# Kernel optimization log

Measured on AMD Instinct MI355X. Metric: run time of the kernel, lower is better.

The kernel has to match this reference:

```python
import jax, jax.numpy as jnp
import numpy as np

NUM_HEADS = 16


def _rotate_half(x):
    x1, x2 = jnp.split(x, 2, axis=-1)
    return jnp.concatenate([-x2, x1], axis=-1)


def _rope_apply(x, sin, cos):
    return x * cos + _rotate_half(x) * sin


def setup_inputs() -> dict:
    key = jax.random.key(0)
    ks = jax.random.split(key, 6)
    B, N, C, HD = 2, 2048, 1024, 64
    x = jax.random.normal(ks[0], (B, N, C), dtype=jnp.float32)
    sin = jax.random.uniform(ks[1], (N - 1, HD), dtype=jnp.float32)
    cos = jax.random.uniform(ks[2], (N - 1, HD), dtype=jnp.float32)
    qkv_w = jax.random.normal(ks[3], (3 * C, C), dtype=jnp.float32) * (C ** -0.5)
    proj_w = jax.random.normal(ks[4], (C, C), dtype=jnp.float32) * (C ** -0.5)
    proj_b = jax.random.normal(ks[5], (C,), dtype=jnp.float32) * 0.02
    return {"x": x, "sin": sin, "cos": cos, "qkv_w": qkv_w,
            "proj_w": proj_w, "proj_b": proj_b}


def reference(x, sin, cos, qkv_w, proj_w, proj_b):
    B, N, C = x.shape
    H = NUM_HEADS
    hd = C // H
    scale = hd ** -0.5

    # QKV projection (no bias): [B,N,3C] -> [B,N,3,H,hd]
    qkv = jnp.einsum('bnc,dc->bnd', x, qkv_w).reshape(B, N, 3, H, hd)
    q = qkv[:, :, 0].transpose(0, 2, 1, 3)  # [B,H,N,hd]
    k = qkv[:, :, 1].transpose(0, 2, 1, 3)
    v = qkv[:, :, 2].transpose(0, 2, 1, 3)

    # RoPE with prefix tokens left unrotated
    prefix = N - sin.shape[0]
    q = jnp.concatenate([q[:, :, :prefix], _rope_apply(q[:, :, prefix:], sin, cos)], axis=2)
    k = jnp.concatenate([k[:, :, :prefix], _rope_apply(k[:, :, prefix:], sin, cos)], axis=2)

    # SDPA (non-causal, no mask)
    scores = jnp.einsum('bhqd,bhkd->bhqk', q, k) * scale
    attn = jax.nn.softmax(scores, axis=-1)
    o = jnp.einsum('bhqk,bhkd->bhqd', attn, v)  # [B,H,N,hd]
    o = o.transpose(0, 2, 1, 3).reshape(B, N, C)

    # Output projection
    return jnp.einsum('bnc,dc->bnd', o, proj_w) + proj_b
```

## Files before the change

kernel.cpp:

```cpp
#include <hip/hip_runtime.h>
#include <hip/hip_bf16.h>
#include <stdint.h>

typedef __hip_bfloat16 bf16;
typedef __attribute__((ext_vector_type(8))) short short8;
typedef __attribute__((ext_vector_type(4))) float floatx4;

#define DEVI static __device__ __forceinline__

typedef __attribute__((address_space(1))) const uint32_t gu32;
typedef __attribute__((address_space(3))) uint32_t lu32;

DEVI void gld_lds16(const void* g, void* l) {
    __builtin_amdgcn_global_load_lds((gu32*)g, (lu32*)l, 16, 0, 0);
}

#define QSCALE 0.18033688011112042f
#define SM_SHIFT 16.0f

__global__ void cvt3_bf16_kernel(const float* __restrict__ s0, bf16* __restrict__ d0, int n0,
                                 const float* __restrict__ s1, bf16* __restrict__ d1, int n1,
                                 const float* __restrict__ s2, bf16* __restrict__ d2, int n2) {
    int c = blockIdx.x * 256 + threadIdx.x;
    const float* src; bf16* dst;
    if (c < n0)           { src = s0; dst = d0; }
    else if (c < n0 + n1) { src = s1; dst = d1; c -= n0; }
    else if (c < n0 + n1 + n2) { src = s2; dst = d2; c -= n0 + n1; }
    else return;
    const int i = c * 4;
    float4 v = *(const float4*)(src + i);
    union { bf16 h[4]; uint2 u; } o;
    o.h[0] = __float2bfloat16(v.x);
    o.h[1] = __float2bfloat16(v.y);
    o.h[2] = __float2bfloat16(v.z);
    o.h[3] = __float2bfloat16(v.w);
    *(uint2*)(dst + i) = o.u;
}

template<int BM, int OUT_BF16, int ADD_BIAS, int SCALE_Q, int ROPE>
__global__ __launch_bounds__(256, 2) void gemm_bt_kernel(
    const bf16* __restrict__ A, const bf16* __restrict__ Bt,
    const float* __restrict__ bias, const float* __restrict__ sinp,
    const float* __restrict__ cosp, void* __restrict__ Cout,
    int M, int N, int K, int nbn)
{
    constexpr int BK = 32;
    constexpr int MFRAG = BM / 32;
    __shared__ __align__(16) bf16 As[BM * BK];
    __shared__ __align__(16) bf16 Bs[128 * BK];
    const int sb = (blockIdx.x & 7) * ((int)gridDim.x >> 3) + (blockIdx.x >> 3);
    const int bm = sb / nbn;
    const int bn = sb % nbn;
    const int lane = threadIdx.x & 63;
    const int wave = threadIdx.x >> 6;
    const int wm = (wave >> 1) * (BM / 2);
    const int wn = (wave & 1) << 6;

    const int srow0 = wave * 16 + (lane >> 2);
    const int skc = (lane & 3) * 8;
    const bf16* Ap0 = A + (size_t)(bm * BM + srow0) * K + skc;
    const bf16* Ap1 = A + (size_t)(bm * BM + srow0 + 64) * K + skc;
    const bf16* Bp0 = Bt + (size_t)(bn * 128 + srow0) * K + skc;
    const bf16* Bp1 = Bt + (size_t)(bn * 128 + srow0 + 64) * K + skc;
    bf16* As0 = &As[wave * 512];
    bf16* As1 = &As[wave * 512 + 2048];
    bf16* Bs0 = &Bs[wave * 512];
    bf16* Bs1 = &Bs[wave * 512 + 2048];

    const int frow = lane & 15;
    const int fk   = (lane >> 4) * 8;

    floatx4 acc[MFRAG][4] = {};

    for (int kt = 0; kt < K; kt += BK) {
        gld_lds16(Ap0 + kt, As0);
        if (BM == 128) gld_lds16(Ap1 + kt, As1);
        gld_lds16(Bp0 + kt, Bs0);
        gld_lds16(Bp1 + kt, Bs1);
        __syncthreads();
        short8 af[MFRAG], bfv[4];
#pragma unroll
        for (int m = 0; m < MFRAG; ++m) af[m] = *(const short8*)&As[(wm + m * 16 + frow) * BK + fk];
#pragma unroll
        for (int n = 0; n < 4; ++n) bfv[n] = *(const short8*)&Bs[(wn + n * 16 + frow) * BK + fk];
#pragma unroll
        for (int m = 0; m < MFRAG; ++m)
#pragma unroll
            for (int n = 0; n < 4; ++n)
                acc[m][n] = __builtin_amdgcn_mfma_f32_16x16x32_bf16(af[m], bfv[n], acc[m][n], 0, 0, 0);
        __syncthreads();
    }

    const int rbase = bm * BM + wm + (lane >> 4) * 4;
    const int cbase = bn * 128 + wn + frow;
#pragma unroll
    for (int m = 0; m < MFRAG; ++m)
#pragma unroll
        for (int r = 0; r < 4; ++r) {
            const int row = rbase + m * 16 + r;
            if (ROPE) {
                const int ntok = row & 2047;
                const int n1 = ntok - 1;
#pragma unroll
                for (int p = 0; p < 2; ++p) {
                    const int colA = cbase + p * 16;
                    const float qs = (SCALE_Q && colA < 1024) ? QSCALE : 1.0f;
                    float vA = acc[m][p][r] * qs;
                    float vB = acc[m][p + 2][r] * qs;
                    if (colA < 2048 && ntok >= 1) {
                        const int j = colA & 63;
                        const int sc = n1 * 64 + j;
                        const float c1 = cosp[sc],      s1 = sinp[sc];
                        const float c2 = cosp[sc + 32], s2 = sinp[sc + 32];
                        const float oA = vA * c1 - vB * s1;
                        const float oB = vB * c2 + vA * s2;
                        vA = oA; vB = oB;
                    }
                    const size_t ia = (size_t)row * N + colA;
                    ((bf16*)Cout)[ia]      = __float2bfloat16(vA);
                    ((bf16*)Cout)[ia + 32] = __float2bfloat16(vB);
                }
            } else {
#pragma unroll
                for (int n = 0; n < 4; ++n) {
                    const int col = cbase + n * 16;
                    const float bv = ADD_BIAS ? bias[col] : 0.f;
                    const float v = acc[m][n][r] + bv;
                    const size_t idx = (size_t)row * N + col;
                    if (OUT_BF16) ((bf16*)Cout)[idx] = __float2bfloat16(v);
                    else          ((float*)Cout)[idx] = v;
                }
            }
        }
}

__global__ __launch_bounds__(512, 4) void attn_kernel(const bf16* __restrict__ qkv,
                                                      bf16* __restrict__ O) {
    __shared__ __align__(16) bf16 Ks[2][64 * 64];
    __shared__ __align__(16) bf16 Vt[2][64 * 64];

    const int bid = blockIdx.x;
    const int bh = bid & 31;
    const int qt = bid >> 5;
    const int b = bh >> 4;
    const int h = bh & 15;
    const int lane = threadIdx.x & 63;
    const int wave = threadIdx.x >> 6;
    const int t = threadIdx.x;

    const bf16* qb = qkv + (size_t)b * 2048 * 3072 + h * 64;
    const bf16* kb = qb + 1024;
    const bf16* vb = qb + 2048;

    const int frow = lane & 15;
    const int ks   = lane >> 4;
    const int q0   = qt * 128 + wave * 16;

    const bf16* qr = qb + (size_t)(q0 + frow) * 3072;
    const short8 qf0 = *(const short8*)(qr + ks * 8);
    const short8 qf1 = *(const short8*)(qr + 32 + ks * 8);

    short8 vfo = {};
    if (frow == 0) {
        const short one = (short)0x3F80;
#pragma unroll
        for (int j = 0; j < 8; ++j) vfo[j] = one;
    }

    const bool vrole = (wave < 4);

    const int kidx = (wave & 3) * 64 + lane;
    const int kr0 = kidx >> 3, kr1 = (kidx + 256) >> 3;
    const bf16* Kp0 = kb + (size_t)kr0 * 3072 + (((kidx & 7) ^ (kr0 & 7)) * 8);
    const bf16* Kp1 = kb + (size_t)kr1 * 3072 + (((kidx & 7) ^ (kr1 & 7)) * 8);

    const int vkt = wave & 3;
    const int vg  = (t >> 4) & 3;
    const int cb  = t & 15;
    const bf16* Vp = vb + (size_t)(vkt * 16 + vg * 4) * 3072 + cb * 4;
    const int vc = vg + ((vkt >> 1) << 2);
    const int vr = (vkt & 1) * 4;

    floatx4 acc[4] = {};
    floatx4 acc_s = {};

    union VU { ushort4 v; unsigned short e[4]; };
    VU vv[4];

    auto stage_issue = [&](int k0, int buf) {
        if (vrole) {
#pragma unroll
            for (int i = 0; i < 4; ++i)
                vv[i].v = *(const ushort4*)(Vp + (size_t)(k0 + i) * 3072);
        } else {
            gld_lds16(Kp0 + (size_t)k0 * 3072, &Ks[buf][(wave & 3) * 512]);
            gld_lds16(Kp1 + (size_t)k0 * 3072, &Ks[buf][(wave & 3) * 512 + 2048]);
        }
    };
    auto stage_write = [&](int buf) {
        if (vrole) {
#pragma unroll
            for (int j = 0; j < 4; ++j) {
                union { unsigned short u[4]; unsigned long long ll; } pk;
#pragma unroll
                for (int i = 0; i < 4; ++i) pk.u[i] = vv[i].e[j];
                const int d = cb * 4 + j;
                const int s = ((d >> 2) & 7) ^ ((d & 3) << 1);
                *(unsigned long long*)&Vt[buf][d * 64 + (((vc ^ s) << 3) + vr)] = pk.ll;
            }
        }
    };

    stage_issue(0, 0);
    stage_write(0);
    __syncthreads();

    for (int tt = 0; tt < 32; ++tt) {
        const int cur = tt & 1;
        if (tt < 31) stage_issue((tt + 1) * 64, cur ^ 1);

        short8 kf0[4], kf1[4];
#pragma unroll
        for (int kt = 0; kt < 4; ++kt) {
            const int row = kt * 16 + frow;
            kf0[kt] = *(const short8*)&Ks[cur][row * 64 + ((ks ^ (row & 7)) * 8)];
            kf1[kt] = *(const short8*)&Ks[cur][row * 64 + (((ks + 4) ^ (row & 7)) * 8)];
        }
        short8 vf0[4], vf1[4];
#pragma unroll
        for (int dt = 0; dt < 4; ++dt) {
            const int d = dt * 16 + frow;
            const int s = ((d >> 2) & 7) ^ ((d & 3) << 1);
            vf0[dt] = *(const short8*)&Vt[cur][d * 64 + ((ks ^ s) << 3)];
            vf1[dt] = *(const short8*)&Vt[cur][d * 64 + (((ks + 4) ^ s) << 3)];
        }

        floatx4 sv[4];
        __builtin_amdgcn_s_setprio(1);
#pragma unroll
        for (int kt = 0; kt < 4; ++kt) {
            floatx4 z = {-SM_SHIFT, -SM_SHIFT, -SM_SHIFT, -SM_SHIFT};
            z = __builtin_amdgcn_mfma_f32_16x16x32_bf16(kf0[kt], qf0, z, 0, 0, 0);
            z = __builtin_amdgcn_mfma_f32_16x16x32_bf16(kf1[kt], qf1, z, 0, 0, 0);
            sv[kt] = z;
        }
        __builtin_amdgcn_s_setprio(0);

        union PU { __hip_bfloat162 h2[4]; short8 v; };
        PU p0, p1;
#pragma unroll
        for (int kt = 0; kt < 4; ++kt)
#pragma unroll
            for (int m = 0; m < 2; ++m) {
                const float a = __builtin_amdgcn_exp2f(sv[kt][2 * m]);
                const float c = __builtin_amdgcn_exp2f(sv[kt][2 * m + 1]);
                const __hip_bfloat162 pk = __float22bfloat162_rn(float2{a, c});
                if (kt < 2) p0.h2[kt * 2 + m] = pk;
                else        p1.h2[(kt - 2) * 2 + m] = pk;
            }

        __builtin_amdgcn_s_setprio(1);
#pragma unroll
        for (int dt = 0; dt < 4; ++dt) {
            acc[dt] = __builtin_amdgcn_mfma_f32_16x16x32_bf16(p0.v, vf0[dt], acc[dt], 0, 0, 0);
            acc[dt] = __builtin_amdgcn_mfma_f32_16x16x32_bf16(p1.v, vf1[dt], acc[dt], 0, 0, 0);
        }
        acc_s = __builtin_amdgcn_mfma_f32_16x16x32_bf16(p0.v, vfo, acc_s, 0, 0, 0);
        acc_s = __builtin_amdgcn_mfma_f32_16x16x32_bf16(p1.v, vfo, acc_s, 0, 0, 0);
        __builtin_amdgcn_s_setprio(0);

        if (tt < 31) stage_write(cur ^ 1);
        __syncthreads();
    }

    floatx4 li;
#pragma unroll
    for (int i = 0; i < 4; ++i) li[i] = 1.0f / __shfl(acc_s[i], lane & 48);
    const int nrow = q0 + (lane >> 4) * 4;
#pragma unroll
    for (int i = 0; i < 4; ++i) {
        const size_t base = ((size_t)b * 2048 + nrow + i) * 1024 + h * 64 + frow;
#pragma unroll
        for (int dt = 0; dt < 4; ++dt)
            O[base + dt * 16] = __float2bfloat16(acc[dt][i] * li[i]);
    }
}

extern "C" void kernel_launch(void* const* d_in, const int* in_sizes, int n_in,
                              void* d_out, int out_size, void* d_ws, size_t ws_size,
                              hipStream_t stream) {
    const float* x      = (const float*)d_in[0];
    const float* sinp   = (const float*)d_in[1];
    const float* cosp   = (const float*)d_in[2];
    const float* qkv_w  = (const float*)d_in[3];
    const float* proj_w = (const float*)d_in[4];
    const float* proj_b = (const float*)d_in[5];
    float* out = (float*)d_out;

    char* ws = (char*)d_ws;
    bf16* xb    = (bf16*)(ws);
    bf16* wqkv  = (bf16*)(ws + 8388608);
    bf16* wproj = (bf16*)(ws + 8388608 + 6291456);
    bf16* qkvb  = (bf16*)(ws + 16777216);
    bf16* attno = (bf16*)(ws + 16777216 + 25165824);

    cvt3_bf16_kernel<<<(1048576 + 786432 + 262144) / 256, 256, 0, stream>>>(
        x, xb, 1048576, qkv_w, wqkv, 786432, proj_w, wproj, 262144);

    gemm_bt_kernel<128, 1, 0, 1, 1><<<32 * 24, 256, 0, stream>>>(
        xb, wqkv, nullptr, sinp, cosp, qkvb, 4096, 3072, 1024, 24);
    attn_kernel<<<512, 512, 0, stream>>>(qkvb, attno);
    gemm_bt_kernel<64, 0, 1, 0, 0><<<64 * 8, 256, 0, stream>>>(
        attno, wproj, proj_b, nullptr, nullptr, out, 4096, 1024, 1024, 8);
}
```

Baseline: 116.1 us.

## Double GEMM K-tile with swizzled LDS and halve attention barriers via 128-key stages

The GEMM K tile grows from 32 to 64 with an XOR-swizzled LDS layout, so each barrier pair covers two MFMA k-steps and bank conflicts are avoided. The attention kernel now stages two 64-key sub-tiles per iteration, with V loads for the second sub-tile interleaved between computations. This halves the number of __syncthreads and loop iterations in both kernels. In exchange it doubles LDS use, which may cut occupancy, and adds register pressure.

Result: slower. 122.3 us (+5.4%).

```diff
diff --git a/kernel.cpp b/kernel.cpp
--- a/kernel.cpp
+++ b/kernel.cpp
@@ -44,8 +44,9 @@
     const float* __restrict__ cosp, void* __restrict__ Cout,
     int M, int N, int K, int nbn)
 {
-    constexpr int BK = 32;
+    constexpr int BK = 64;
     constexpr int MFRAG = BM / 32;
+    constexpr int ALOADS = BM / 32;
     __shared__ __align__(16) bf16 As[BM * BK];
     __shared__ __align__(16) bf16 Bs[128 * BK];
     const int sb = (blockIdx.x & 7) * ((int)gridDim.x >> 3) + (blockIdx.x >> 3);
@@ -56,38 +57,45 @@
     const int wm = (wave >> 1) * (BM / 2);
     const int wn = (wave & 1) << 6;
 
-    const int srow0 = wave * 16 + (lane >> 2);
-    const int skc = (lane & 3) * 8;
-    const bf16* Ap0 = A + (size_t)(bm * BM + srow0) * K + skc;
-    const bf16* Ap1 = A + (size_t)(bm * BM + srow0 + 64) * K + skc;
-    const bf16* Bp0 = Bt + (size_t)(bn * 128 + srow0) * K + skc;
-    const bf16* Bp1 = Bt + (size_t)(bn * 128 + srow0 + 64) * K + skc;
-    bf16* As0 = &As[wave * 512];
-    bf16* As1 = &As[wave * 512 + 2048];
-    bf16* Bs0 = &Bs[wave * 512];
-    bf16* Bs1 = &Bs[wave * 512 + 2048];
+    const int srow = wave * 8 + (lane >> 3);
+    const int skc = (((lane & 7) ^ (lane >> 3)) * 8);
+    const bf16* Ap = A + (size_t)(bm * BM + srow) * K + skc;
+    const bf16* Bp = Bt + (size_t)(bn * 128 + srow) * K + skc;
+    bf16* AsD = &As[wave * 512];
+    bf16* BsD = &Bs[wave * 512];
 
     const int frow = lane & 15;
-    const int fk   = (lane >> 4) * 8;
+    const int ks   = lane >> 4;
 
     floatx4 acc[MFRAG][4] = {};
 
     for (int kt = 0; kt < K; kt += BK) {
-        gld_lds16(Ap0 + kt, As0);
-        if (BM == 128) gld_lds16(Ap1 + kt, As1);
-        gld_lds16(Bp0 + kt, Bs0);
-        gld_lds16(Bp1 + kt, Bs1);
+#pragma unroll
+        for (int s = 0; s < ALOADS; ++s)
+            gld_lds16(Ap + kt + (size_t)(32 * s) * K, AsD + 2048 * s);
+#pragma unroll
+        for (int s = 0; s < 4; ++s)
+            gld_lds16(Bp + kt + (size_t)(32 * s) * K, BsD + 2048 * s);
         __syncthreads();
-        short8 af[MFRAG], bfv[4];
-#pragma unroll
-        for (int m = 0; m < MFRAG; ++m) af[m] = *(const short8*)&As[(wm + m * 16 + frow) * BK + fk];
-#pragma unroll
-        for (int n = 0; n < 4; ++n) bfv[n] = *(const short8*)&Bs[(wn + n * 16 + frow) * BK + fk];
-#pragma unroll
-        for (int m = 0; m < MFRAG; ++m)
-#pragma unroll
-            for (int n = 0; n < 4; ++n)
-                acc[m][n] = __builtin_amdgcn_mfma_f32_16x16x32_bf16(af[m], bfv[n], acc[m][n], 0, 0, 0);
+#pragma unroll
+        for (int half = 0; half < 2; ++half) {
+            short8 af[MFRAG], bfv[4];
+#pragma unroll
+            for (int m = 0; m < MFRAG; ++m) {
+                const int row = wm + m * 16 + frow;
+                af[m] = *(const short8*)&As[row * 64 + (((half * 4 + ks) ^ (row & 7)) * 8)];
+            }
+#pragma unroll
+            for (int n = 0; n < 4; ++n) {
+                const int row = wn + n * 16 + frow;
+                bfv[n] = *(const short8*)&Bs[row * 64 + (((half * 4 + ks) ^ (row & 7)) * 8)];
+            }
+#pragma unroll
+            for (int m = 0; m < MFRAG; ++m)
+#pragma unroll
+                for (int n = 0; n < 4; ++n)
+                    acc[m][n] = __builtin_amdgcn_mfma_f32_16x16x32_bf16(af[m], bfv[n], acc[m][n], 0, 0, 0);
+        }
         __syncthreads();
     }
 
@@ -136,8 +144,8 @@
 
 __global__ __launch_bounds__(512, 4) void attn_kernel(const bf16* __restrict__ qkv,
                                                       bf16* __restrict__ O) {
-    __shared__ __align__(16) bf16 Ks[2][64 * 64];
-    __shared__ __align__(16) bf16 Vt[2][64 * 64];
+    __shared__ __align__(16) bf16 Ks[2][2][64 * 64];
+    __shared__ __align__(16) bf16 Vt[2][2][64 * 64];
 
     const int bid = blockIdx.x;
     const int bh = bid & 31;
@@ -187,52 +195,42 @@
     union VU { ushort4 v; unsigned short e[4]; };
     VU vv[4];
 
-    auto stage_issue = [&](int k0, int buf) {
-        if (vrole) {
-#pragma unroll
-            for (int i = 0; i < 4; ++i)
-                vv[i].v = *(const ushort4*)(Vp + (size_t)(k0 + i) * 3072);
-        } else {
-            gld_lds16(Kp0 + (size_t)k0 * 3072, &Ks[buf][(wave & 3) * 512]);
-            gld_lds16(Kp1 + (size_t)k0 * 3072, &Ks[buf][(wave & 3) * 512 + 2048]);
-        }
+    auto issueV = [&](int k0) {
+#pragma unroll
+        for (int i = 0; i < 4; ++i)
+            vv[i].v = *(const ushort4*)(Vp + (size_t)(k0 + i) * 3072);
     };
-    auto stage_write = [&](int buf) {
-        if (vrole) {
-#pragma unroll
-            for (int j = 0; j < 4; ++j) {
-                union { unsigned short u[4]; unsigned long long ll; } pk;
-#pragma unroll
-                for (int i = 0; i < 4; ++i) pk.u[i] = vv[i].e[j];
-                const int d = cb * 4 + j;
-                const int s = ((d >> 2) & 7) ^ ((d & 3) << 1);
-                *(unsigned long long*)&Vt[buf][d * 64 + (((vc ^ s) << 3) + vr)] = pk.ll;
-            }
+    auto writeV = [&](int buf, int sub) {
+#pragma unroll
+        for (int j = 0; j < 4; ++j) {
+            union { unsigned short u[4]; unsigned long long ll; } pk;
+#pragma unroll
+            for (int i = 0; i < 4; ++i) pk.u[i] = vv[i].e[j];
+            const int d = cb * 4 + j;
+            const int s = ((d >> 2) & 7) ^ ((d & 3) << 1);
+            *(unsigned long long*)&Vt[buf][sub][d * 64 + (((vc ^ s) << 3) + vr)] = pk.ll;
         }
     };
-
-    stage_issue(0, 0);
-    stage_write(0);
-    __syncthreads();
-
-    for (int tt = 0; tt < 32; ++tt) {
-        const int cur = tt & 1;
-        if (tt < 31) stage_issue((tt + 1) * 64, cur ^ 1);
-
+    auto stageK = [&](int k0, int buf, int sub) {
+        gld_lds16(Kp0 + (size_t)k0 * 3072, &Ks[buf][sub][(wave & 3) * 512]);
+        gld_lds16(Kp1 + (size_t)k0 * 3072, &Ks[buf][sub][(wave & 3) * 512 + 2048]);
+    };
+
+    auto compute_tile = [&](int buf, int sub) {
         short8 kf0[4], kf1[4];
 #pragma unroll
         for (int kt = 0; kt < 4; ++kt) {
             const int row = kt * 16 + frow;
-            kf0[kt] = *(const short8*)&Ks[cur][row * 64 + ((ks ^ (row & 7)) * 8)];
-            kf1[kt] = *(const short8*)&Ks[cur][row * 64 + (((ks + 4) ^ (row & 7)) * 8)];
+            kf0[kt] = *(const short8*)&Ks[buf][sub][row * 64 + ((ks ^ (row & 7)) * 8)];
+            kf1[kt] = *(const short8*)&Ks[buf][sub][row * 64 + (((ks + 4) ^ (row & 7)) * 8)];
         }
         short8 vf0[4], vf1[4];
 #pragma unroll
         for (int dt = 0; dt < 4; ++dt) {
             const int d = dt * 16 + frow;
             const int s = ((d >> 2) & 7) ^ ((d & 3) << 1);
-            vf0[dt] = *(const short8*)&Vt[cur][d * 64 + ((ks ^ s) << 3)];
-            vf1[dt] = *(const short8*)&Vt[cur][d * 64 + (((ks + 4) ^ s) << 3)];
+            vf0[dt] = *(const short8*)&Vt[buf][sub][d * 64 + ((ks ^ s) << 3)];
+            vf1[dt] = *(const short8*)&Vt[buf][sub][d * 64 + (((ks + 4) ^ s) << 3)];
         }
 
         floatx4 sv[4];
@@ -268,8 +266,29 @@
         acc_s = __builtin_amdgcn_mfma_f32_16x16x32_bf16(p0.v, vfo, acc_s, 0, 0, 0);
         acc_s = __builtin_amdgcn_mfma_f32_16x16x32_bf16(p1.v, vfo, acc_s, 0, 0, 0);
         __builtin_amdgcn_s_setprio(0);
-
-        if (tt < 31) stage_write(cur ^ 1);
+    };
+
+    if (vrole) {
+        issueV(0);  writeV(0, 0);
+        issueV(64); writeV(0, 1);
+    } else {
+        stageK(0, 0, 0);
+        stageK(64, 0, 1);
+    }
+    __syncthreads();
+
+    for (int tt = 0; tt < 16; ++tt) {
+        const int cur = tt & 1, nxt = cur ^ 1;
+        const int k0 = tt * 128;
+        const bool pf = tt < 15;
+        if (pf) {
+            if (vrole) issueV(k0 + 128);
+            else { stageK(k0 + 128, nxt, 0); stageK(k0 + 192, nxt, 1); }
+        }
+        compute_tile(cur, 0);
+        if (pf && vrole) { writeV(nxt, 0); issueV(k0 + 192); }
+        compute_tile(cur, 1);
+        if (pf && vrole) writeV(nxt, 1);
         __syncthreads();
     }
 
```

## Double GEMM K-tile to 64 and XOR-swizzle LDS layout

Applied to the files above, without the earlier changes.

Raises the GEMM K tile from 32 to 64, so each main-loop iteration loads twice as much data and runs two MFMA half-steps between barriers. This halves the number of __syncthreads pairs and global-to-LDS issue rounds. The LDS tiles are also stored with an XOR swizzle on the 16-byte chunk index to avoid bank conflicts on the fragment reads. The cost is doubled LDS use per block, which may limit occupancy under the 2-blocks-per-CU launch bound.

Measured after the change: 108.5 us (median of 2 runs). -6.6%, faster.

```diff
diff --git a/kernel.cpp b/kernel.cpp
--- a/kernel.cpp
+++ b/kernel.cpp
@@ -44,8 +44,9 @@
     const float* __restrict__ cosp, void* __restrict__ Cout,
     int M, int N, int K, int nbn)
 {
-    constexpr int BK = 32;
+    constexpr int BK = 64;
     constexpr int MFRAG = BM / 32;
+    constexpr int ALOADS = BM / 32;
     __shared__ __align__(16) bf16 As[BM * BK];
     __shared__ __align__(16) bf16 Bs[128 * BK];
     const int sb = (blockIdx.x & 7) * ((int)gridDim.x >> 3) + (blockIdx.x >> 3);
@@ -56,38 +57,45 @@
     const int wm = (wave >> 1) * (BM / 2);
     const int wn = (wave & 1) << 6;
 
-    const int srow0 = wave * 16 + (lane >> 2);
-    const int skc = (lane & 3) * 8;
-    const bf16* Ap0 = A + (size_t)(bm * BM + srow0) * K + skc;
-    const bf16* Ap1 = A + (size_t)(bm * BM + srow0 + 64) * K + skc;
-    const bf16* Bp0 = Bt + (size_t)(bn * 128 + srow0) * K + skc;
-    const bf16* Bp1 = Bt + (size_t)(bn * 128 + srow0 + 64) * K + skc;
-    bf16* As0 = &As[wave * 512];
-    bf16* As1 = &As[wave * 512 + 2048];
-    bf16* Bs0 = &Bs[wave * 512];
-    bf16* Bs1 = &Bs[wave * 512 + 2048];
+    const int srow = wave * 8 + (lane >> 3);
+    const int skc = (((lane & 7) ^ (lane >> 3)) * 8);
+    const bf16* Ap = A + (size_t)(bm * BM + srow) * K + skc;
+    const bf16* Bp = Bt + (size_t)(bn * 128 + srow) * K + skc;
+    bf16* AsD = &As[wave * 512];
+    bf16* BsD = &Bs[wave * 512];
 
     const int frow = lane & 15;
-    const int fk   = (lane >> 4) * 8;
+    const int ks   = lane >> 4;
 
     floatx4 acc[MFRAG][4] = {};
 
     for (int kt = 0; kt < K; kt += BK) {
-        gld_lds16(Ap0 + kt, As0);
-        if (BM == 128) gld_lds16(Ap1 + kt, As1);
-        gld_lds16(Bp0 + kt, Bs0);
-        gld_lds16(Bp1 + kt, Bs1);
+#pragma unroll
+        for (int s = 0; s < ALOADS; ++s)
+            gld_lds16(Ap + kt + (size_t)(32 * s) * K, AsD + 2048 * s);
+#pragma unroll
+        for (int s = 0; s < 4; ++s)
+            gld_lds16(Bp + kt + (size_t)(32 * s) * K, BsD + 2048 * s);
         __syncthreads();
-        short8 af[MFRAG], bfv[4];
-#pragma unroll
-        for (int m = 0; m < MFRAG; ++m) af[m] = *(const short8*)&As[(wm + m * 16 + frow) * BK + fk];
-#pragma unroll
-        for (int n = 0; n < 4; ++n) bfv[n] = *(const short8*)&Bs[(wn + n * 16 + frow) * BK + fk];
-#pragma unroll
-        for (int m = 0; m < MFRAG; ++m)
-#pragma unroll
-            for (int n = 0; n < 4; ++n)
-                acc[m][n] = __builtin_amdgcn_mfma_f32_16x16x32_bf16(af[m], bfv[n], acc[m][n], 0, 0, 0);
+#pragma unroll
+        for (int half = 0; half < 2; ++half) {
+            short8 af[MFRAG], bfv[4];
+#pragma unroll
+            for (int m = 0; m < MFRAG; ++m) {
+                const int row = wm + m * 16 + frow;
+                af[m] = *(const short8*)&As[row * 64 + (((half * 4 + ks) ^ (row & 7)) * 8)];
+            }
+#pragma unroll
+            for (int n = 0; n < 4; ++n) {
+                const int row = wn + n * 16 + frow;
+                bfv[n] = *(const short8*)&Bs[row * 64 + (((half * 4 + ks) ^ (row & 7)) * 8)];
+            }
+#pragma unroll
+            for (int m = 0; m < MFRAG; ++m)
+#pragma unroll
+                for (int n = 0; n < 4; ++n)
+                    acc[m][n] = __builtin_amdgcn_mfma_f32_16x16x32_bf16(af[m], bfv[n], acc[m][n], 0, 0, 0);
+        }
         __syncthreads();
     }
 
```
